# Kernel tuning notes

Hardware: AMD Instinct MI355X
Metric: run time of the kernel (lower is better)

The kernel has to match this reference:

```python
import jax, jax.numpy as jnp
import numpy as np

H, DM, DK, DV = 16, 1024, 64, 64
S, B = 2048, 2


def setup_inputs() -> dict:
    key = jax.random.key(0)
    ks = jax.random.split(key, 7)
    u = 1.0 / np.sqrt(DM)
    uo = 1.0 / np.sqrt(H * DV)
    return {
        "Q": jax.random.normal(ks[0], (S, B, DM), jnp.float32),
        "K": jax.random.normal(ks[1], (S, B, DM), jnp.float32),
        "V": jax.random.normal(ks[2], (S, B, DM), jnp.float32),
        "WQ": jax.random.uniform(ks[3], (H, DM, DK), jnp.float32, -u, u),
        "WK": jax.random.uniform(ks[4], (H, DM, DK), jnp.float32, -u, u),
        "WV": jax.random.uniform(ks[5], (H, DM, DV), jnp.float32, -u, u),
        "WO": jax.random.uniform(ks[6], (H * DV, DM), jnp.float32, -uo, uo),
    }


def reference(Q, K, V, WQ, WK, WV, WO):
    # Layout: (seq, batch, feat); heads stacked as leading dim of weights.
    q = jnp.einsum('sbm,hmk->hsbk', Q, WQ)   # [H,S,B,DK]
    k = jnp.einsum('sbm,hmk->hsbk', K, WK)
    v = jnp.einsum('sbm,hmv->hsbv', V, WV)
    scores = jnp.einsum('hsbk,htbk->hsbt', q, k) / jnp.sqrt(jnp.asarray(DK, q.dtype))
    # Causal mask: key index t > query index s gets -inf (matches triu inf subtract).
    causal = jnp.arange(S)[None, :] > jnp.arange(S)[:, None]  # [S_q, S_k]
    scores = jnp.where(causal[None, :, None, :], -jnp.inf, scores)
    p = jax.nn.softmax(scores, axis=-1)
    o = jnp.einsum('hsbt,htbv->hsbv', p, v)  # [H,S,B,DV]
    y = jnp.transpose(o, (1, 2, 0, 3)).reshape(S, B, H * DV)  # concat heads on dim 2
    return y @ WO  # [S,B,DM]
```

## Files before the change

kernel.cpp:

```cpp
#include <hip/hip_runtime.h>
#include <hip/hip_bf16.h>


typedef __bf16 bf16;
typedef bf16 bf16x8 __attribute__((ext_vector_type(8)));
typedef float f32x4 __attribute__((ext_vector_type(4)));

#define MFMA16(a, b, c) __builtin_amdgcn_mfma_f32_16x16x32_bf16((a), (b), (c), 0, 0, 0)

typedef bf16 bf16x8_t __attribute__((ext_vector_type(8)));

static __device__ __forceinline__ bf16x8 load8(const bf16* p) {
  return *reinterpret_cast<const bf16x8*>(p);
}
static __device__ __forceinline__ void store8(bf16* p, bf16x8 v) {
  *reinterpret_cast<bf16x8*>(p) = v;
}
static __device__ __forceinline__ bf16x8 cvt8(float4 a, float4 b) {
  bf16x8 o;
  o[0] = (bf16)a.x; o[1] = (bf16)a.y; o[2] = (bf16)a.z; o[3] = (bf16)a.w;
  o[4] = (bf16)b.x; o[5] = (bf16)b.y; o[6] = (bf16)b.z; o[7] = (bf16)b.w;
  return o;
}
static __device__ __forceinline__ f32x4 zero4() {
  f32x4 v; v[0] = 0.f; v[1] = 0.f; v[2] = 0.f; v[3] = 0.f; return v;
}
static __device__ __forceinline__ void gload_lds16(const bf16* g, bf16* l) {
  __builtin_amdgcn_global_load_lds(
      (const __attribute__((address_space(1))) void*)g,
      (__attribute__((address_space(3))) void*)l, 16, 0, 0);
}

__global__ __launch_bounds__(256) void wcvt_kernel(const float* __restrict__ WQ,
                                                   const float* __restrict__ WK,
                                                   const float* __restrict__ WV,
                                                   bf16* __restrict__ out) {
  __shared__ float tile[32][33];
  const int zz = blockIdx.z;
  const int tau = zz >> 4;
  const float* in = ((tau == 0) ? WQ : (tau == 1) ? WK : WV) + (size_t)(zz & 15) * 65536;
  bf16* o = out + (size_t)zz * 65536;
  const float scale = (tau == 0) ? 0.125f * 1.44269504f : 1.0f;
  const int r0 = blockIdx.y * 32, c0 = blockIdx.x * 32;
  const int tx = threadIdx.x & 31, ty = threadIdx.x >> 5;
#pragma unroll
  for (int i = 0; i < 32; i += 8) tile[ty + i][tx] = in[(size_t)(r0 + ty + i) * 64 + c0 + tx];
  __syncthreads();
#pragma unroll
  for (int i = 0; i < 32; i += 8)
    o[(size_t)(c0 + ty + i) * 1024 + r0 + tx] = (bf16)(tile[tx][ty + i] * scale);
}

__global__ __launch_bounds__(256) void tcvt_kernel(const float* __restrict__ in,
                                                   bf16* __restrict__ out, int R, int C) {
  __shared__ float tile[32][33];
  const int r0 = blockIdx.y * 32, c0 = blockIdx.x * 32;
  const int tx = threadIdx.x & 31, ty = threadIdx.x >> 5;
#pragma unroll
  for (int i = 0; i < 32; i += 8) tile[ty + i][tx] = in[(size_t)(r0 + ty + i) * C + c0 + tx];
  __syncthreads();
#pragma unroll
  for (int i = 0; i < 32; i += 8)
    out[(size_t)(c0 + ty + i) * R + r0 + tx] = (bf16)tile[tx][ty + i];
}

__global__ __launch_bounds__(256) void proj_kernel(
    const float* __restrict__ X0, const float* __restrict__ X1, const float* __restrict__ X2,
    const bf16* __restrict__ Wt, bf16* __restrict__ qws, bf16* __restrict__ kws,
    bf16* __restrict__ vtws) {
  const int id = blockIdx.x;
  const int n = id / 96;
  const int w = id % 96;
  const int z = w >> 5;
  const int m = w & 31;
  const float* X = (z == 0) ? X0 : ((z == 1) ? X1 : X2);
  const bf16* Wz = Wt + (size_t)z * 1024 * 1024;
  const int mBase = m * 128;
  const int nBase = n * 128;

  __shared__ bf16 Al[2][128][40];
  __shared__ bf16 Bl[2][128 * 32];

  const int t = threadIdx.x;
  const int lane = t & 63;
  const int wave = t >> 6;
  const int wm = (wave >> 1) * 64;
  const int wn = (wave & 1) * 64;
  const int ln = lane & 15;
  const int quad = lane >> 4;
  const int bswz = quad ^ ((ln >> 1) & 3);

  f32x4 acc[4][4];
#pragma unroll
  for (int i = 0; i < 4; i++)
#pragma unroll
    for (int j = 0; j < 4; j++) acc[i][j] = zero4();

  const int ar = t >> 1;
  const int ak = (t & 1) * 16;
  const float4* Abase = reinterpret_cast<const float4*>(X + (size_t)(mBase + ar) * 1024 + ak);

  float4 pv[4];
#pragma unroll
  for (int i = 0; i < 4; i++) pv[i] = Abase[i];
#pragma unroll
  for (int i = 0; i < 2; i++) {
    const int c = i * 256 + t;
    const int mp = c >> 2;
    const int ql = (c & 3) ^ ((mp >> 1) & 3);
    gload_lds16(Wz + (size_t)(nBase + mp) * 1024 + ql * 8, &Bl[0][(i * 256 + wave * 64) * 8]);
  }
  store8(&Al[0][ar][ak], cvt8(pv[0], pv[1]));
  store8(&Al[0][ar][ak + 8], cvt8(pv[2], pv[3]));
  __syncthreads();

  for (int k0 = 0; k0 < 1024; k0 += 32) {
    const int cur = (k0 >> 5) & 1, nxt = cur ^ 1;
    const bool more = (k0 + 32) < 1024;
    if (more) {
      const int kn = (k0 + 32) >> 2;
#pragma unroll
      for (int i = 0; i < 4; i++) pv[i] = Abase[kn + i];
#pragma unroll
      for (int i = 0; i < 2; i++) {
        const int c = i * 256 + t;
        const int mp = c >> 2;
        const int ql = (c & 3) ^ ((mp >> 1) & 3);
        gload_lds16(Wz + (size_t)(nBase + mp) * 1024 + k0 + 32 + ql * 8,
                    &Bl[nxt][(i * 256 + wave * 64) * 8]);
      }
    }
    bf16x8 a[4], bfr[4];
#pragma unroll
    for (int i = 0; i < 4; i++) a[i] = load8(&Al[cur][wm + i * 16 + ln][quad * 8]);
#pragma unroll
    for (int j = 0; j < 4; j++) bfr[j] = load8(&Bl[cur][((wn + j * 16 + ln) * 4 + bswz) * 8]);
#pragma unroll
    for (int i = 0; i < 4; i++)
#pragma unroll
      for (int j = 0; j < 4; j++) acc[i][j] = MFMA16(a[i], bfr[j], acc[i][j]);
    if (more) {
      store8(&Al[nxt][ar][ak], cvt8(pv[0], pv[1]));
      store8(&Al[nxt][ar][ak + 8], cvt8(pv[2], pv[3]));
    }
    __syncthreads();
  }

#pragma unroll
  for (int i = 0; i < 4; i++) {
#pragma unroll
    for (int j = 0; j < 4; j++) {
      const int col = nBase + wn + j * 16 + ln;
      const int h = col >> 6, d = col & 63;
#pragma unroll
      for (int r = 0; r < 4; r++) {
        const int row = mBase + wm + i * 16 + quad * 4 + r;
        const int s = row >> 1, bb = row & 1;
        const int hb = h * 2 + bb;
        const bf16 val = (bf16)acc[i][j][r];
        if (z == 0) {
          qws[((size_t)hb * 2048 + s) * 64 + d] = val;
        } else if (z == 1) {
          kws[((size_t)hb * 2048 + s) * 64 + d] = val;
        } else {
          const int pos = ((s >> 7) << 7) + ((s & 15) << 3) + ((s >> 4) & 7);
          vtws[((size_t)hb * 64 + d) * 2048 + pos] = val;
        }
      }
    }
  }
}

__global__ __launch_bounds__(256) void attn_kernel(
    const bf16* __restrict__ qws, const bf16* __restrict__ kws, const bf16* __restrict__ vtws,
    bf16* __restrict__ cc) {
  const int id = blockIdx.x;
  const int hb = id & 31;
  const int p = id >> 5;
  const int h = hb >> 1, b = hb & 1;

  const int t = threadIdx.x;
  const int lane = t & 63;
  const int wave = t >> 6;
  const int ln = lane & 15;
  const int quad = lane >> 4;
  const int swz3 = ln & 7;

  const bf16* qh = qws + (size_t)hb * 2048 * 64;
  const bf16* kh = kws + (size_t)hb * 2048 * 64;
  const bf16* vh = vtws + (size_t)hb * 64 * 2048;

  __shared__ bf16 Kl[2][128 * 64];
  __shared__ bf16 Vl[2][64 * 128];
  __shared__ bf16 Pl[4 * 32 * 128];
  bf16* Plw = Pl + (size_t)wave * 32 * 128;

  bf16x8 ones;
#pragma unroll
  for (int i = 0; i < 8; i++) ones[i] = (bf16)1.0f;

  const int kmp = t >> 3, kq = (t & 7) ^ (kmp & 7);
  const int vdp = t >> 4, vq = (t & 15) ^ (vdp & 7);

#pragma unroll
  for (int seg = 0; seg < 2; seg++) {
    const int qb = seg ? (15 - p) : p;
    const int q0 = qb * 128;

    bf16x8 qf[2][2];
#pragma unroll
    for (int mb = 0; mb < 2; mb++)
#pragma unroll
      for (int hh = 0; hh < 2; hh++)
        qf[mb][hh] =
            load8(qh + (size_t)(q0 + wave * 32 + mb * 16 + ln) * 64 + hh * 32 + quad * 8);

    f32x4 accO[2][4];
    f32x4 accL[2];
#pragma unroll
    for (int mb = 0; mb < 2; mb++) {
      accL[mb] = zero4();
#pragma unroll
      for (int d = 0; d < 4; d++) accO[mb][d] = zero4();
    }

    __syncthreads();
#pragma unroll
    for (int i = 0; i < 4; i++) {
      const int c256 = (i * 256 + wave * 64) * 8;
      gload_lds16(kh + (size_t)(i * 32 + kmp) * 64 + kq * 8, &Kl[0][c256]);
      gload_lds16(vh + (size_t)(i * 16 + vdp) * 2048 + vq * 8, &Vl[0][c256]);
    }

    for (int jt = 0; jt <= qb; jt++) {
      const int kt0 = jt * 128;
      const int cur = jt & 1, nxt = cur ^ 1;
      __syncthreads();
      if (jt < qb) {
        const int nt0 = kt0 + 128;
#pragma unroll
        for (int i = 0; i < 4; i++) {
          const int c256 = (i * 256 + wave * 64) * 8;
          gload_lds16(kh + (size_t)(nt0 + i * 32 + kmp) * 64 + kq * 8, &Kl[nxt][c256]);
          gload_lds16(vh + (size_t)(i * 16 + vdp) * 2048 + nt0 + vq * 8, &Vl[nxt][c256]);
        }
      }

      f32x4 sv[2][8];
#pragma unroll
      for (int nt = 0; nt < 8; nt++) {
        const int mm = nt * 16 + ln;
        bf16x8 b0 = load8(&Kl[cur][(mm * 8 + (quad ^ swz3)) * 8]);
        bf16x8 b1 = load8(&Kl[cur][(mm * 8 + ((quad + 4) ^ swz3)) * 8]);
#pragma unroll
        for (int mb = 0; mb < 2; mb++) {
          f32x4 s = MFMA16(qf[mb][0], b0, zero4());
          s = MFMA16(qf[mb][1], b1, s);
          sv[mb][nt] = s;
        }
      }
      if (jt == qb) {
#pragma unroll
        for (int mb = 0; mb < 2; mb++)
#pragma unroll
          for (int nt = 0; nt < 8; nt++) {
            const int kg = kt0 + nt * 16 + ln;
#pragma unroll
            for (int r = 0; r < 4; r++) {
              const int qg = q0 + wave * 32 + mb * 16 + quad * 4 + r;
              if (kg > qg) sv[mb][nt][r] = -1e30f;
            }
          }
      }
#pragma unroll
      for (int mb = 0; mb < 2; mb++) {
#pragma unroll
        for (int r = 0; r < 4; r++) {
          const int row = mb * 16 + quad * 4 + r;
          bf16x8 pw;
#pragma unroll
          for (int nt = 0; nt < 8; nt++) pw[nt] = (bf16)exp2f(sv[mb][nt][r]);
          store8(Plw + (size_t)(row * 16 + (ln ^ (row & 7))) * 8, pw);
        }
      }
#pragma unroll
      for (int ks = 0; ks < 4; ks++) {
        bf16x8 pa[2];
#pragma unroll
        for (int mb = 0; mb < 2; mb++) {
          const int row = mb * 16 + ln;
          pa[mb] = load8(Plw + (size_t)(row * 16 + ((ks * 4 + quad) ^ (ln & 7))) * 8);
        }
#pragma unroll
        for (int d = 0; d < 4; d++) {
          const int drow = d * 16 + ln;
          bf16x8 vb = load8(&Vl[cur][(drow * 16 + ((ks * 4 + quad) ^ swz3)) * 8]);
#pragma unroll
          for (int mb = 0; mb < 2; mb++) accO[mb][d] = MFMA16(pa[mb], vb, accO[mb][d]);
        }
#pragma unroll
        for (int mb = 0; mb < 2; mb++) accL[mb] = MFMA16(pa[mb], ones, accL[mb]);
      }
    }

#pragma unroll
    for (int mb = 0; mb < 2; mb++) {
#pragma unroll
      for (int r = 0; r < 4; r++) {
        const float inv = 1.0f / accL[mb][r];
        const int s = q0 + wave * 32 + mb * 16 + quad * 4 + r;
#pragma unroll
        for (int d = 0; d < 4; d++)
          cc[((size_t)s * 2 + b) * 1024 + h * 64 + d * 16 + ln] = (bf16)(accO[mb][d][r] * inv);
      }
    }
  }
}

__global__ __launch_bounds__(256) void out_kernel(
    const bf16* __restrict__ A, const bf16* __restrict__ Bt, float* __restrict__ outp) {
  const int id = blockIdx.x;
  const int nb = id >> 6;
  const int mb = id & 63;
  const int mBase = mb * 64, nBase = nb * 128;

  __shared__ bf16 Al[2][64 * 32];
  __shared__ bf16 Bl[2][128 * 32];

  const int t = threadIdx.x;
  const int lane = t & 63;
  const int wave = t >> 6;
  const int wm = (wave >> 1) * 32;
  const int wn = (wave & 1) * 64;
  const int ln = lane & 15;
  const int quad = lane >> 4;
  const int bswz = quad ^ ((ln >> 1) & 3);

  f32x4 acc[2][4];
#pragma unroll
  for (int i = 0; i < 2; i++)
#pragma unroll
    for (int j = 0; j < 4; j++) acc[i][j] = zero4();

  const int amp = t >> 2, aql = (t & 3) ^ ((amp >> 1) & 3);

  gload_lds16(A + (size_t)(mBase + amp) * 1024 + aql * 8, &Al[0][(wave * 64) * 8]);
#pragma unroll
  for (int i = 0; i < 2; i++) {
    const int c = i * 256 + t;
    const int mp = c >> 2, ql = (c & 3) ^ ((mp >> 1) & 3);
    gload_lds16(Bt + (size_t)(nBase + mp) * 1024 + ql * 8, &Bl[0][(i * 256 + wave * 64) * 8]);
  }
  __syncthreads();

  for (int k0 = 0; k0 < 1024; k0 += 32) {
    const int cur = (k0 >> 5) & 1, nxt = cur ^ 1;
    const bool more = (k0 + 32) < 1024;
    if (more) {
      gload_lds16(A + (size_t)(mBase + amp) * 1024 + k0 + 32 + aql * 8, &Al[nxt][(wave * 64) * 8]);
#pragma unroll
      for (int i = 0; i < 2; i++) {
        const int c = i * 256 + t;
        const int mp = c >> 2, ql = (c & 3) ^ ((mp >> 1) & 3);
        gload_lds16(Bt + (size_t)(nBase + mp) * 1024 + k0 + 32 + ql * 8,
                    &Bl[nxt][(i * 256 + wave * 64) * 8]);
      }
    }
    bf16x8 a[2], bfr[4];
#pragma unroll
    for (int i = 0; i < 2; i++) a[i] = load8(&Al[cur][((wm + i * 16 + ln) * 4 + bswz) * 8]);
#pragma unroll
    for (int jj = 0; jj < 4; jj++) bfr[jj] = load8(&Bl[cur][((wn + jj * 16 + ln) * 4 + bswz) * 8]);
#pragma unroll
    for (int i = 0; i < 2; i++)
#pragma unroll
      for (int jj = 0; jj < 4; jj++) acc[i][jj] = MFMA16(a[i], bfr[jj], acc[i][jj]);
    __syncthreads();
  }

#pragma unroll
  for (int i = 0; i < 2; i++)
#pragma unroll
    for (int jj = 0; jj < 4; jj++)
#pragma unroll
      for (int r = 0; r < 4; r++)
        outp[(size_t)(mBase + wm + i * 16 + quad * 4 + r) * 1024 + nBase + wn + jj * 16 + ln] =
            acc[i][jj][r];
}

extern "C" void kernel_launch(void* const* d_in, const int* in_sizes, int n_in,
                              void* d_out, int out_size, void* d_ws, size_t ws_size,
                              hipStream_t stream) {
  (void)in_sizes; (void)n_in; (void)out_size; (void)ws_size;
  const float* Q  = (const float*)d_in[0];
  const float* K  = (const float*)d_in[1];
  const float* V  = (const float*)d_in[2];
  const float* WQ = (const float*)d_in[3];
  const float* WK = (const float*)d_in[4];
  const float* WV = (const float*)d_in[5];
  const float* WO = (const float*)d_in[6];
  float* outp = (float*)d_out;

  const size_t REG = (size_t)4 * 1024 * 1024;
  bf16* base = (bf16*)d_ws;
  bf16* Wt   = base;
  bf16* cc   = base;
  bf16* qws  = base + REG;
  bf16* WOt  = base + REG;
  bf16* kws  = base + 2 * REG;
  bf16* vtws = base + 3 * REG;

  wcvt_kernel<<<dim3(2, 32, 48), 256, 0, stream>>>(WQ, WK, WV, Wt);
  proj_kernel<<<dim3(768), 256, 0, stream>>>(Q, K, V, Wt, qws, kws, vtws);
  attn_kernel<<<dim3(256), 256, 0, stream>>>(qws, kws, vtws, cc);
  tcvt_kernel<<<dim3(32, 32, 1), 256, 0, stream>>>(WO, WOt, 1024, 1024);
  out_kernel<<<dim3(8 * 64), 256, 0, stream>>>(cc, WOt, outp);
}
```

Baseline: 240.4 us.

## Split attention into one block per query tile with 64-key tiles and direct V loads

The attention kernel no longer pairs two query tiles per block. It launches 512 blocks, one per query tile, scheduled heaviest-first, and sets launch bounds for three blocks per CU. Key tiles shrink from 128 to 64 rows. V fragments are now read straight from global memory in a new 64-wide interleaved layout written by the projection kernel, so V is no longer staged in LDS, which cuts shared memory use. The intent is more occupancy and parallelism. The cost is uneven per-block work, more loop iterations and barriers, and uncached global V loads on the critical path.

```diff
diff --git a/kernel.cpp b/kernel.cpp
--- a/kernel.cpp
+++ b/kernel.cpp
@@ -4,17 +4,19 @@
 
 typedef __bf16 bf16;
 typedef bf16 bf16x8 __attribute__((ext_vector_type(8)));
+typedef bf16 bf16x4 __attribute__((ext_vector_type(4)));
 typedef float f32x4 __attribute__((ext_vector_type(4)));
 
 #define MFMA16(a, b, c) __builtin_amdgcn_mfma_f32_16x16x32_bf16((a), (b), (c), 0, 0, 0)
-
-typedef bf16 bf16x8_t __attribute__((ext_vector_type(8)));
 
 static __device__ __forceinline__ bf16x8 load8(const bf16* p) {
   return *reinterpret_cast<const bf16x8*>(p);
 }
 static __device__ __forceinline__ void store8(bf16* p, bf16x8 v) {
   *reinterpret_cast<bf16x8*>(p) = v;
+}
+static __device__ __forceinline__ void store4(bf16* p, bf16x4 v) {
+  *reinterpret_cast<bf16x4*>(p) = v;
 }
 static __device__ __forceinline__ bf16x8 cvt8(float4 a, float4 b) {
   bf16x8 o;
@@ -163,7 +165,7 @@
         } else if (z == 1) {
           kws[((size_t)hb * 2048 + s) * 64 + d] = val;
         } else {
-          const int pos = ((s >> 7) << 7) + ((s & 15) << 3) + ((s >> 4) & 7);
+          const int pos = (s & ~63) | ((s & 15) << 2) | ((s >> 4) & 3);
           vtws[((size_t)hb * 64 + d) * 2048 + pos] = val;
         }
       }
@@ -171,12 +173,13 @@
   }
 }
 
-__global__ __launch_bounds__(256) void attn_kernel(
+__global__ __launch_bounds__(256, 3) void attn_kernel(
     const bf16* __restrict__ qws, const bf16* __restrict__ kws, const bf16* __restrict__ vtws,
     bf16* __restrict__ cc) {
   const int id = blockIdx.x;
   const int hb = id & 31;
-  const int p = id >> 5;
+  const int qb = 15 - (id >> 5);
+  const int q0 = qb * 128;
   const int h = hb >> 1, b = hb & 1;
 
   const int t = threadIdx.x;
@@ -190,129 +193,125 @@
   const bf16* kh = kws + (size_t)hb * 2048 * 64;
   const bf16* vh = vtws + (size_t)hb * 64 * 2048;
 
-  __shared__ bf16 Kl[2][128 * 64];
-  __shared__ bf16 Vl[2][64 * 128];
-  __shared__ bf16 Pl[4 * 32 * 128];
-  bf16* Plw = Pl + (size_t)wave * 32 * 128;
+  __shared__ bf16 Kl[2][64 * 64];
+  __shared__ bf16 Pl[4][32 * 72];
+  bf16* Plw = &Pl[wave][0];
 
   bf16x8 ones;
 #pragma unroll
   for (int i = 0; i < 8; i++) ones[i] = (bf16)1.0f;
 
-  const int kmp = t >> 3, kq = (t & 7) ^ (kmp & 7);
-  const int vdp = t >> 4, vq = (t & 15) ^ (vdp & 7);
-
-#pragma unroll
-  for (int seg = 0; seg < 2; seg++) {
-    const int qb = seg ? (15 - p) : p;
-    const int q0 = qb * 128;
-
-    bf16x8 qf[2][2];
-#pragma unroll
-    for (int mb = 0; mb < 2; mb++)
-#pragma unroll
-      for (int hh = 0; hh < 2; hh++)
-        qf[mb][hh] =
-            load8(qh + (size_t)(q0 + wave * 32 + mb * 16 + ln) * 64 + hh * 32 + quad * 8);
-
-    f32x4 accO[2][4];
-    f32x4 accL[2];
+  bf16x8 qf[2][2];
+#pragma unroll
+  for (int mb = 0; mb < 2; mb++)
+#pragma unroll
+    for (int hh = 0; hh < 2; hh++)
+      qf[mb][hh] = load8(qh + (size_t)(q0 + wave * 32 + mb * 16 + ln) * 64 + hh * 32 + quad * 8);
+
+  f32x4 accO[2][4];
+  f32x4 accL[2];
+#pragma unroll
+  for (int mb = 0; mb < 2; mb++) {
+    accL[mb] = zero4();
+#pragma unroll
+    for (int d = 0; d < 4; d++) accO[mb][d] = zero4();
+  }
+
+#pragma unroll
+  for (int i = 0; i < 2; i++) {
+    const int c = i * 256 + t;
+    const int mp = c >> 3;
+    const int ql = (c & 7) ^ (mp & 7);
+    gload_lds16(kh + (size_t)mp * 64 + ql * 8, &Kl[0][(i * 256 + wave * 64) * 8]);
+  }
+
+  const int Jmax = 2 * qb + 2;
+  for (int jt = 0; jt < Jmax; jt++) {
+    const int kt0 = jt * 64;
+    const int cur = jt & 1, nxt = cur ^ 1;
+    __syncthreads();
+    if (jt + 1 < Jmax) {
+      const int nt0 = kt0 + 64;
+#pragma unroll
+      for (int i = 0; i < 2; i++) {
+        const int c = i * 256 + t;
+        const int mp = c >> 3;
+        const int ql = (c & 7) ^ (mp & 7);
+        gload_lds16(kh + (size_t)(nt0 + mp) * 64 + ql * 8, &Kl[nxt][(i * 256 + wave * 64) * 8]);
+      }
+    }
+
+    f32x4 sv[2][4];
+#pragma unroll
+    for (int nt = 0; nt < 4; nt++) {
+      const int mm = nt * 16 + ln;
+      bf16x8 b0 = load8(&Kl[cur][(mm * 8 + (quad ^ swz3)) * 8]);
+      bf16x8 b1 = load8(&Kl[cur][(mm * 8 + ((quad + 4) ^ swz3)) * 8]);
+#pragma unroll
+      for (int mb = 0; mb < 2; mb++) {
+        f32x4 s = MFMA16(qf[mb][0], b0, zero4());
+        s = MFMA16(qf[mb][1], b1, s);
+        sv[mb][nt] = s;
+      }
+    }
+
+    bf16x8 vb[2][4];
+#pragma unroll
+    for (int ks = 0; ks < 2; ks++)
+#pragma unroll
+      for (int d = 0; d < 4; d++)
+        vb[ks][d] = load8(vh + (size_t)(d * 16 + ln) * 2048 + kt0 + (ks * 4 + quad) * 8);
+
+    if (jt >= 2 * qb) {
+#pragma unroll
+      for (int mb = 0; mb < 2; mb++)
+#pragma unroll
+        for (int nt = 0; nt < 4; nt++) {
+          const int kg = kt0 + nt * 16 + ln;
+#pragma unroll
+          for (int r = 0; r < 4; r++) {
+            const int qg = q0 + wave * 32 + mb * 16 + quad * 4 + r;
+            if (kg > qg) sv[mb][nt][r] = -1e30f;
+          }
+        }
+    }
+
 #pragma unroll
     for (int mb = 0; mb < 2; mb++) {
-      accL[mb] = zero4();
-#pragma unroll
-      for (int d = 0; d < 4; d++) accO[mb][d] = zero4();
-    }
-
-    __syncthreads();
-#pragma unroll
-    for (int i = 0; i < 4; i++) {
-      const int c256 = (i * 256 + wave * 64) * 8;
-      gload_lds16(kh + (size_t)(i * 32 + kmp) * 64 + kq * 8, &Kl[0][c256]);
-      gload_lds16(vh + (size_t)(i * 16 + vdp) * 2048 + vq * 8, &Vl[0][c256]);
-    }
-
-    for (int jt = 0; jt <= qb; jt++) {
-      const int kt0 = jt * 128;
-      const int cur = jt & 1, nxt = cur ^ 1;
-      __syncthreads();
-      if (jt < qb) {
-        const int nt0 = kt0 + 128;
-#pragma unroll
-        for (int i = 0; i < 4; i++) {
-          const int c256 = (i * 256 + wave * 64) * 8;
-          gload_lds16(kh + (size_t)(nt0 + i * 32 + kmp) * 64 + kq * 8, &Kl[nxt][c256]);
-          gload_lds16(vh + (size_t)(i * 16 + vdp) * 2048 + nt0 + vq * 8, &Vl[nxt][c256]);
-        }
-      }
-
-      f32x4 sv[2][8];
-#pragma unroll
-      for (int nt = 0; nt < 8; nt++) {
-        const int mm = nt * 16 + ln;
-        bf16x8 b0 = load8(&Kl[cur][(mm * 8 + (quad ^ swz3)) * 8]);
-        bf16x8 b1 = load8(&Kl[cur][(mm * 8 + ((quad + 4) ^ swz3)) * 8]);
-#pragma unroll
-        for (int mb = 0; mb < 2; mb++) {
-          f32x4 s = MFMA16(qf[mb][0], b0, zero4());
-          s = MFMA16(qf[mb][1], b1, s);
-          sv[mb][nt] = s;
-        }
-      }
-      if (jt == qb) {
-#pragma unroll
-        for (int mb = 0; mb < 2; mb++)
-#pragma unroll
-          for (int nt = 0; nt < 8; nt++) {
-            const int kg = kt0 + nt * 16 + ln;
-#pragma unroll
-            for (int r = 0; r < 4; r++) {
-              const int qg = q0 + wave * 32 + mb * 16 + quad * 4 + r;
-              if (kg > qg) sv[mb][nt][r] = -1e30f;
-            }
-          }
-      }
-#pragma unroll
-      for (int mb = 0; mb < 2; mb++) {
-#pragma unroll
-        for (int r = 0; r < 4; r++) {
-          const int row = mb * 16 + quad * 4 + r;
-          bf16x8 pw;
-#pragma unroll
-          for (int nt = 0; nt < 8; nt++) pw[nt] = (bf16)exp2f(sv[mb][nt][r]);
-          store8(Plw + (size_t)(row * 16 + (ln ^ (row & 7))) * 8, pw);
-        }
-      }
-#pragma unroll
-      for (int ks = 0; ks < 4; ks++) {
-        bf16x8 pa[2];
-#pragma unroll
-        for (int mb = 0; mb < 2; mb++) {
-          const int row = mb * 16 + ln;
-          pa[mb] = load8(Plw + (size_t)(row * 16 + ((ks * 4 + quad) ^ (ln & 7))) * 8);
-        }
-#pragma unroll
-        for (int d = 0; d < 4; d++) {
-          const int drow = d * 16 + ln;
-          bf16x8 vb = load8(&Vl[cur][(drow * 16 + ((ks * 4 + quad) ^ swz3)) * 8]);
-#pragma unroll
-          for (int mb = 0; mb < 2; mb++) accO[mb][d] = MFMA16(pa[mb], vb, accO[mb][d]);
-        }
-#pragma unroll
-        for (int mb = 0; mb < 2; mb++) accL[mb] = MFMA16(pa[mb], ones, accL[mb]);
-      }
-    }
-
-#pragma unroll
-    for (int mb = 0; mb < 2; mb++) {
 #pragma unroll
       for (int r = 0; r < 4; r++) {
-        const float inv = 1.0f / accL[mb][r];
-        const int s = q0 + wave * 32 + mb * 16 + quad * 4 + r;
-#pragma unroll
-        for (int d = 0; d < 4; d++)
-          cc[((size_t)s * 2 + b) * 1024 + h * 64 + d * 16 + ln] = (bf16)(accO[mb][d][r] * inv);
-      }
+        const int row = mb * 16 + quad * 4 + r;
+        bf16x4 pw;
+#pragma unroll
+        for (int nt = 0; nt < 4; nt++) pw[nt] = (bf16)exp2f(sv[mb][nt][r]);
+        store4(Plw + row * 72 + ln * 4, pw);
+      }
+    }
+
+#pragma unroll
+    for (int ks = 0; ks < 2; ks++) {
+      bf16x8 pa[2];
+#pragma unroll
+      for (int mb = 0; mb < 2; mb++)
+        pa[mb] = load8(Plw + (mb * 16 + ln) * 72 + (ks * 4 + quad) * 8);
+#pragma unroll
+      for (int d = 0; d < 4; d++)
+#pragma unroll
+        for (int mb = 0; mb < 2; mb++) accO[mb][d] = MFMA16(pa[mb], vb[ks][d], accO[mb][d]);
+#pragma unroll
+      for (int mb = 0; mb < 2; mb++) accL[mb] = MFMA16(pa[mb], ones, accL[mb]);
+    }
+  }
+
+#pragma unroll
+  for (int mb = 0; mb < 2; mb++) {
+#pragma unroll
+    for (int r = 0; r < 4; r++) {
+      const float inv = 1.0f / accL[mb][r];
+      const int s = q0 + wave * 32 + mb * 16 + quad * 4 + r;
+#pragma unroll
+      for (int d = 0; d < 4; d++)
+        cc[((size_t)s * 2 + b) * 1024 + h * 64 + d * 16 + ln] = (bf16)(accO[mb][d][r] * inv);
     }
   }
 }
@@ -412,7 +411,7 @@
 
   wcvt_kernel<<<dim3(2, 32, 48), 256, 0, stream>>>(WQ, WK, WV, Wt);
   proj_kernel<<<dim3(768), 256, 0, stream>>>(Q, K, V, Wt, qws, kws, vtws);
-  attn_kernel<<<dim3(256), 256, 0, stream>>>(qws, kws, vtws, cc);
+  attn_kernel<<<dim3(512), 256, 0, stream>>>(qws, kws, vtws, cc);
   tcvt_kernel<<<dim3(32, 32, 1), 256, 0, stream>>>(WO, WOt, 1024, 1024);
   out_kernel<<<dim3(8 * 64), 256, 0, stream>>>(cc, WOt, outp);
 }
```

Result: no change. 243.4 us (+1.2%).
